# Kernel optimization log

Measured on AMD Instinct MI355X. Metric: run time of the kernel, lower is better.

The kernel has to match this reference:

```python
import jax, jax.numpy as jnp
import numpy as np
from jax import lax

B, H, W, CIN = 16, 224, 224, 8
F = 256            # filter_inpt feature dim
K = 3              # ksize (square)
NC = 16            # n_channels (output channels)
NP = CIN * NC * K * K  # 1152 dynamic filter params per sample


def setup_inputs() -> dict:
    key = jax.random.key(0)
    ks = jax.random.split(key, 8)
    s_in = 1.0 / np.sqrt(F)
    return {
        "inpt": jax.random.normal(ks[0], (B, H, W, CIN), jnp.float32),
        "filter_inpt": jax.random.normal(ks[1], (B, F), jnp.float32),
        # param_layer_1 (ELU affine, F -> F)
        "W1": jax.random.normal(ks[2], (F, F), jnp.float32) * s_in,
        "b1": jnp.zeros((F,), jnp.float32),
        # dynamic_weights affine (F -> NP), uniform_unit_scaling(0.1)-like scale
        "Wd": jax.random.normal(ks[3], (F, NP), jnp.float32) * (0.1 * s_in),
        "bd": jnp.zeros((NP,), jnp.float32),
        # dynamic_bias affine (F -> NC), scale sqrt(2)
        "Wb": jax.random.normal(ks[4], (F, NC), jnp.float32) * (np.sqrt(2.0) * s_in),
        "bb": jnp.zeros((NC,), jnp.float32),
        # static learned bias (1,1,1,NC)
        "dfn_bias": jax.random.normal(ks[5], (1, 1, 1, NC), jnp.float32) * 0.01,
    }


def reference(inpt, filter_inpt, W1, b1, Wd, bd, Wb, bb, dfn_bias):
    # param layers: (n_param_layers - 1) = 1 ELU affine keeping width F
    h = jax.nn.elu(filter_inpt @ W1 + b1)                      # [B, F]
    dyn = h @ Wd + bd                                          # [B, CIN*NC*K*K]
    # per-sample filter, ordered (Cin, kh, kw, out_ch) to match patch layout below
    w = dyn.reshape(B, CIN * K * K, NC)                        # [B, P, NC]
    # im2col patches: conv_general_dilated_patches on NCHW -> [B, CIN*K*K, H, W]
    patches = lax.conv_general_dilated_patches(
        jnp.transpose(inpt, (0, 3, 1, 2)), (K, K), (1, 1), 'SAME')
    patches = jnp.transpose(patches, (0, 2, 3, 1))             # [B, H, W, P]
    out = jnp.einsum('bhwp,bpc->bhwc', patches, w)             # [B, H, W, NC]
    # adaptive (per-sample) bias + static bias
    out = out + (h @ Wb + bb)[:, None, None, :] + dfn_bias
    return jax.nn.elu(out)
```

## Files before the change

### kernel.cpp

```cpp
#include <hip/hip_runtime.h>
#include <math.h>

constexpr int BN  = 16;
constexpr int HH  = 224;
constexpr int WW  = 224;
constexpr int CI  = 8;
constexpr int FF  = 256;
constexpr int NC  = 16;
constexpr int NP  = 1152;

typedef __attribute__((ext_vector_type(8))) short short8;
typedef __attribute__((ext_vector_type(4))) float f32x4;

__device__ __forceinline__ float elu_f(float x) {
    return x > 0.0f ? x : (__expf(x) - 1.0f);
}

__device__ __forceinline__ void split8(const float* v, short8& hi, short8& lo) {
#pragma unroll
    for (int j = 0; j < 8; ++j) {
        const unsigned u = __float_as_uint(v[j]);
        hi[j] = (short)(u >> 16);
        const float hf = __uint_as_float(u & 0xffff0000u);
        lo[j] = (short)(__float_as_uint(v[j] - hf) >> 16);
    }
}

__global__ __launch_bounds__(128) void k_h(const float* __restrict__ fi,
                                           const float* __restrict__ W1,
                                           const float* __restrict__ b1,
                                           const float* __restrict__ bd,
                                           const float* __restrict__ bb,
                                           const float* __restrict__ dfn,
                                           float* __restrict__ h_out,
                                           float* __restrict__ w_out,
                                           float* __restrict__ bias_out) {
    __shared__ float x[FF];
    int bid = blockIdx.x;
    int b = bid >> 1, half = bid & 1;
    int t = threadIdx.x;
    x[t]       = fi[b * FF + t];
    x[t + 128] = fi[b * FF + t + 128];
    __syncthreads();
    int col = half * 128 + t;
    float acc = b1[col];
#pragma unroll 8
    for (int k = 0; k < FF; ++k) acc = fmaf(x[k], W1[k * FF + col], acc);
    h_out[b * FF + col] = elu_f(acc);

    const int gid = bid * 128 + t;
    for (int i = gid; i < BN * NP; i += 4096) {
        const int c = i - (i / NP) * NP;
        w_out[i] = bd[c];
    }
    if (gid < BN * NC) bias_out[gid] = bb[gid & 15] + dfn[gid & 15];
}

__global__ __launch_bounds__(128) void k_dyn(const float* __restrict__ h_in,
                                             const float* __restrict__ Wd,
                                             const float* __restrict__ Wb,
                                             float* __restrict__ w_out,
                                             float* __restrict__ bias_out) {
    __shared__ float hs[16][32];
    const int bid = blockIdx.x;
    const int cg  = bid % 9;
    const int ks  = bid / 9;
    const int k0  = ks * 32;
    const int t   = threadIdx.x;

#pragma unroll
    for (int j = 0; j < 4; ++j) {
        const int idx = t + 128 * j;
        const int bi = idx >> 5, kk = idx & 31;
        hs[bi][kk] = h_in[bi * FF + k0 + kk];
    }
    __syncthreads();

    const int i = cg * 128 + t;
    float a[16];
#pragma unroll
    for (int b = 0; b < 16; ++b) a[b] = 0.0f;

#pragma unroll 8
    for (int kk = 0; kk < 32; ++kk) {
        const float w = Wd[(size_t)(k0 + kk) * NP + i];
#pragma unroll
        for (int b = 0; b < 16; ++b) a[b] = fmaf(hs[b][kk], w, a[b]);
    }
#pragma unroll
    for (int b = 0; b < 16; ++b) atomicAdd(&w_out[b * NP + i], a[b]);

    if (cg == 0) {
#pragma unroll
        for (int r = 0; r < 2; ++r) {
            const int p = t + r * 128;
            const int b = p >> 4, c = p & 15;
            float s = 0.0f;
#pragma unroll 8
            for (int kk = 0; kk < 32; ++kk)
                s = fmaf(hs[b][kk], Wb[(size_t)(k0 + kk) * NC + c], s);
            atomicAdd(&bias_out[b * NC + c], s);
        }
    }
}

__global__ __launch_bounds__(128) void k_conv(const float* __restrict__ in,
                                              const float* __restrict__ w_all,
                                              const float* __restrict__ bias_all,
                                              float* __restrict__ out) {
    const int b    = blockIdx.z;
    const int half = blockIdx.x;
    const int t    = threadIdx.x;
    const int wid  = t >> 6;
    const int lane = t & 63;
    const int cl   = lane & 15;
    const int g    = lane >> 4;
    const int y    = blockIdx.y * 2 + wid;

    int  dyL[3], dxL[3];
    bool real[3];
#pragma unroll
    for (int c = 0; c < 3; ++c) {
        const int tap = c * 4 + g;
        real[c] = (tap < 9);
        const int tp = real[c] ? tap : 0;
        dyL[c] = tp / 3;
        dxL[c] = tp - 3 * dyL[c];
    }

    const float* __restrict__ wq = w_all + b * NP;
    short8 bhi0, blo0, bhi1, blo1, bhi2, blo2;
    {
        float wv[8];
#pragma unroll
        for (int i = 0; i < 8; ++i)
            wv[i] = real[0] ? wq[(i * 9 + (0 * 4 + g)) * NC + cl] : 0.0f;
        split8(wv, bhi0, blo0);
#pragma unroll
        for (int i = 0; i < 8; ++i)
            wv[i] = real[1] ? wq[(i * 9 + (1 * 4 + g)) * NC + cl] : 0.0f;
        split8(wv, bhi1, blo1);
#pragma unroll
        for (int i = 0; i < 8; ++i)
            wv[i] = real[2] ? wq[(i * 9 + (2 * 4 + g)) * NC + cl] : 0.0f;
        split8(wv, bhi2, blo2);
    }

    size_t ro[3];
    bool   okr[3];
#pragma unroll
    for (int c = 0; c < 3; ++c) {
        const int iy = y + dyL[c] - 1;
        okr[c] = real[c] && ((unsigned)iy < (unsigned)HH);
        const int iyc = min(max(iy, 0), HH - 1);
        ro[c] = ((size_t)(b * HH + iyc) * WW) * CI;
    }

    const float bias = bias_all[b * NC + cl];
    const size_t orow = ((size_t)(b * HH + y) * WW) * NC;

#pragma unroll 1
    for (int tx = 0; tx < 7; ++tx) {
        const int x0 = (half * 7 + tx) * 16;
        f32x4 accM = {bias, bias, bias, bias};
        f32x4 accL = {0.f, 0.f, 0.f, 0.f};
        f32x4 accH = {0.f, 0.f, 0.f, 0.f};

#pragma unroll
        for (int c = 0; c < 3; ++c) {
            const int  ix = x0 + cl + dxL[c] - 1;
            const bool ok = okr[c] && ((unsigned)ix < (unsigned)WW);
            const int  ixc = min(max(ix, 0), WW - 1);
            const float4* pp = (const float4*)(in + ro[c] + (size_t)ixc * CI);
            const float4 a0 = pp[0];
            const float4 a1 = pp[1];
            float av[8];
            av[0] = ok ? a0.x : 0.0f;
            av[1] = ok ? a0.y : 0.0f;
            av[2] = ok ? a0.z : 0.0f;
            av[3] = ok ? a0.w : 0.0f;
            av[4] = ok ? a1.x : 0.0f;
            av[5] = ok ? a1.y : 0.0f;
            av[6] = ok ? a1.z : 0.0f;
            av[7] = ok ? a1.w : 0.0f;
            short8 ahi, alo;
            split8(av, ahi, alo);
            const short8 bh = (c == 0) ? bhi0 : (c == 1) ? bhi1 : bhi2;
            const short8 bl = (c == 0) ? blo0 : (c == 1) ? blo1 : blo2;
            accM = __builtin_amdgcn_mfma_f32_16x16x32_bf16(ahi, bh, accM, 0, 0, 0);
            accL = __builtin_amdgcn_mfma_f32_16x16x32_bf16(alo, bh, accL, 0, 0, 0);
            accH = __builtin_amdgcn_mfma_f32_16x16x32_bf16(ahi, bl, accH, 0, 0, 0);
        }

#pragma unroll
        for (int r = 0; r < 4; ++r) {
            const int px = g * 4 + r;
            out[orow + (size_t)(x0 + px) * NC + cl] =
                elu_f(accM[r] + accL[r] + accH[r]);
        }
    }
}

extern "C" void kernel_launch(void* const* d_in, const int* in_sizes, int n_in,
                              void* d_out, int out_size, void* d_ws, size_t ws_size,
                              hipStream_t stream) {
    const float* inpt = (const float*)d_in[0];
    const float* fi   = (const float*)d_in[1];
    const float* W1   = (const float*)d_in[2];
    const float* b1   = (const float*)d_in[3];
    const float* Wd   = (const float*)d_in[4];
    const float* bd   = (const float*)d_in[5];
    const float* Wb   = (const float*)d_in[6];
    const float* bb   = (const float*)d_in[7];
    const float* dfn  = (const float*)d_in[8];
    float* out = (float*)d_out;

    float* ws    = (float*)d_ws;
    float* h     = ws;
    float* wDyn  = ws + 4096;
    float* biasA = ws + 4096 + 18432;

    k_h  <<<32, 128, 0, stream>>>(fi, W1, b1, bd, bb, dfn, h, wDyn, biasA);
    k_dyn<<<72, 128, 0, stream>>>(h, Wd, Wb, wDyn, biasA);
    k_conv<<<dim3(2, 112, BN), 128, 0, stream>>>(inpt, wDyn, biasA, out);
}
```

Baseline: 46.09 us.

## Prefetch next tile's input in conv loop and remap blocks across XCDs

The conv kernel's inner loop now issues the input loads for the next 16-pixel tile before running the MFMAs on the current tile. A sched_barrier keeps the compiler from sinking those loads, so memory latency overlaps with compute. The flat block id is also permuted so that consecutive rows of one sample land on the same XCD, aiming for better L2 locality on the row halo reuse. This costs extra registers and one redundant load on the final iteration.

```diff
diff --git a/kernel.cpp b/kernel.cpp
--- a/kernel.cpp
+++ b/kernel.cpp
@@ -108,14 +108,19 @@
                                               const float* __restrict__ w_all,
                                               const float* __restrict__ bias_all,
                                               float* __restrict__ out) {
-    const int b    = blockIdx.z;
-    const int half = blockIdx.x;
+    const int hid = blockIdx.x + 2 * (blockIdx.y + 112 * blockIdx.z);
+    const int lid = (hid & 7) * 448 + (hid >> 3);
+    const int b    = lid / 224;
+    const int rem  = lid - b * 224;
+    const int yblk = rem >> 1;
+    const int half = rem & 1;
+
     const int t    = threadIdx.x;
     const int wid  = t >> 6;
     const int lane = t & 63;
     const int cl   = lane & 15;
     const int g    = lane >> 4;
-    const int y    = blockIdx.y * 2 + wid;
+    const int y    = yblk * 2 + wid;
 
     int  dyL[3], dxL[3];
     bool real[3];
@@ -159,9 +164,50 @@
     const float bias = bias_all[b * NC + cl];
     const size_t orow = ((size_t)(b * HH + y) * WW) * NC;
 
+    float4 a00, a01, a10, a11, a20, a21;
+    {
+        const int x0 = (half * 7) * 16;
+#pragma unroll
+        for (int c = 0; c < 3; ++c) {
+            const int ix  = x0 + cl + dxL[c] - 1;
+            const int ixc = min(max(ix, 0), WW - 1);
+            const float4* pp = (const float4*)(in + ro[c] + (size_t)ixc * CI);
+            if (c == 0) { a00 = pp[0]; a01 = pp[1]; }
+            if (c == 1) { a10 = pp[0]; a11 = pp[1]; }
+            if (c == 2) { a20 = pp[0]; a21 = pp[1]; }
+        }
+    }
+
 #pragma unroll 1
     for (int tx = 0; tx < 7; ++tx) {
-        const int x0 = (half * 7 + tx) * 16;
+        const int x0  = (half * 7 + tx) * 16;
+        const int txn = (tx < 6) ? tx + 1 : 6;
+        const int x0n = (half * 7 + txn) * 16;
+
+        const float4 u00 = a00, u01 = a01;
+        const float4 u10 = a10, u11 = a11;
+        const float4 u20 = a20, u21 = a21;
+
+        {
+            const int ix  = x0n + cl + dxL[0] - 1;
+            const int ixc = min(max(ix, 0), WW - 1);
+            const float4* pp = (const float4*)(in + ro[0] + (size_t)ixc * CI);
+            a00 = pp[0]; a01 = pp[1];
+        }
+        {
+            const int ix  = x0n + cl + dxL[1] - 1;
+            const int ixc = min(max(ix, 0), WW - 1);
+            const float4* pp = (const float4*)(in + ro[1] + (size_t)ixc * CI);
+            a10 = pp[0]; a11 = pp[1];
+        }
+        {
+            const int ix  = x0n + cl + dxL[2] - 1;
+            const int ixc = min(max(ix, 0), WW - 1);
+            const float4* pp = (const float4*)(in + ro[2] + (size_t)ixc * CI);
+            a20 = pp[0]; a21 = pp[1];
+        }
+        __builtin_amdgcn_sched_barrier(0);
+
         f32x4 accM = {bias, bias, bias, bias};
         f32x4 accL = {0.f, 0.f, 0.f, 0.f};
         f32x4 accH = {0.f, 0.f, 0.f, 0.f};
@@ -170,19 +216,17 @@
         for (int c = 0; c < 3; ++c) {
             const int  ix = x0 + cl + dxL[c] - 1;
             const bool ok = okr[c] && ((unsigned)ix < (unsigned)WW);
-            const int  ixc = min(max(ix, 0), WW - 1);
-            const float4* pp = (const float4*)(in + ro[c] + (size_t)ixc * CI);
-            const float4 a0 = pp[0];
-            const float4 a1 = pp[1];
+            const float4 v0 = (c == 0) ? u00 : (c == 1) ? u10 : u20;
+            const float4 v1 = (c == 0) ? u01 : (c == 1) ? u11 : u21;
             float av[8];
-            av[0] = ok ? a0.x : 0.0f;
-            av[1] = ok ? a0.y : 0.0f;
-            av[2] = ok ? a0.z : 0.0f;
-            av[3] = ok ? a0.w : 0.0f;
-            av[4] = ok ? a1.x : 0.0f;
-            av[5] = ok ? a1.y : 0.0f;
-            av[6] = ok ? a1.z : 0.0f;
-            av[7] = ok ? a1.w : 0.0f;
+            av[0] = ok ? v0.x : 0.0f;
+            av[1] = ok ? v0.y : 0.0f;
+            av[2] = ok ? v0.z : 0.0f;
+            av[3] = ok ? v0.w : 0.0f;
+            av[4] = ok ? v1.x : 0.0f;
+            av[5] = ok ? v1.y : 0.0f;
+            av[6] = ok ? v1.z : 0.0f;
+            av[7] = ok ? v1.w : 0.0f;
             short8 ahi, alo;
             split8(av, ahi, alo);
             const short8 bh = (c == 0) ? bhi0 : (c == 1) ? bhi1 : bhi2;
```

New measurement: 46.06 us. Within noise of the previous version (-0.1%).
